# Kernel tuning notes

Hardware: AMD Instinct MI355X
Metric: run time of the kernel (lower is better)

The kernel has to match this reference:

```python
import jax, jax.numpy as jnp
import numpy as np

HEADS, DHEAD = 8, 32
INNER = HEADS * DHEAD  # 256


def _conv3x3(x, w, b):
    y = jax.lax.conv_general_dilated(x, w, (1, 1), ((1, 1), (1, 1)),
                                     dimension_numbers=('NCHW', 'OIHW', 'NCHW'))
    return y + b[None, :, None, None]


def _conv1x1(x, w, b):
    return jnp.einsum('oc,bchw->bohw', w, x) + b[None, :, None, None]


def setup_inputs() -> dict:
    key = jax.random.key(0)
    ks = jax.random.split(key, 16)
    s = 0.02
    return {
        'x': jax.random.normal(ks[0], (2, 256, 48, 48), jnp.float32),
        'luma': jax.random.uniform(ks[1], (2, 1, 48, 48), jnp.float32),
        'w_qkv': jax.random.normal(ks[2], (768, 256), jnp.float32) * s,
        'b_qkv': jax.random.normal(ks[3], (768,), jnp.float32) * s,
        'w_proj': jax.random.normal(ks[4], (256, 256), jnp.float32) * s,
        'b_proj': jax.random.normal(ks[5], (256,), jnp.float32) * s,
        'w_c1': jax.random.normal(ks[6], (128, 1, 3, 3), jnp.float32) * s,
        'b_c1': jax.random.normal(ks[7], (128,), jnp.float32) * s,
        'w_c2': jax.random.normal(ks[8], (128, 128, 3, 3), jnp.float32) * s,
        'b_c2': jax.random.normal(ks[9], (128,), jnp.float32) * s,
        'w_g': jax.random.normal(ks[10], (256, 128), jnp.float32) * s,
        'b_g': jax.random.normal(ks[11], (256,), jnp.float32) * s,
        'w_bt': jax.random.normal(ks[12], (256, 128), jnp.float32) * s,
        'b_bt': jax.random.normal(ks[13], (256,), jnp.float32) * s,
        'alpha': jax.random.normal(ks[14], (), jnp.float32) * 0.1,
    }


def reference(x, luma, w_qkv, b_qkv, w_proj, b_proj, w_c1, b_c1, w_c2, b_c2,
              w_g, b_g, w_bt, b_bt, alpha):
    B, C, H, W = x.shape
    N = H * W
    scale = DHEAD ** -0.5

    def to_heads(t):  # [B, h*d, H, W] -> [B, h, N, d]
        return t.reshape(B, HEADS, DHEAD, N).transpose(0, 1, 3, 2)

    qkv = _conv1x1(x, w_qkv, b_qkv)
    q = to_heads(qkv[:, 0 * INNER:1 * INNER])
    k = to_heads(qkv[:, 1 * INNER:2 * INNER])
    v = to_heads(qkv[:, 2 * INNER:3 * INNER])

    # luma conditioning net
    h = jax.nn.relu(_conv3x3(luma, w_c1, b_c1))
    h = jax.nn.relu(_conv3x3(h, w_c2, b_c2))
    gamma = to_heads(_conv1x1(h, w_g, b_g))
    beta = to_heads(_conv1x1(h, w_bt, b_bt))
    q = gamma * q + beta
    k = gamma * k + beta
    v = gamma * v + beta

    # luminance bias: avg_pool2d(3, stride=1, pad=1, count_include_pad=True)
    invL = 1.0 - luma
    invL = jax.lax.reduce_window(invL, 0.0, jax.lax.add, (1, 1, 3, 3), (1, 1, 1, 1),
                                 ((0, 0), (0, 0), (1, 1), (1, 1))) / 9.0
    invL = invL.reshape(B, N)
    invL = invL - invL.mean(axis=-1, keepdims=True)
    q = q + alpha * invL[:, None, :, None]

    attn = jax.nn.softmax(jnp.einsum('bhid,bhjd->bhij', q, k) * scale, axis=-1)
    out = jnp.einsum('bhij,bhjd->bhid', attn, v)
    out = out.transpose(0, 1, 3, 2).reshape(B, INNER, H, W)
    return _conv1x1(out, w_proj, b_proj)
```

## Files before the change

kernel.cpp:

```cpp
#include <hip/hip_runtime.h>
#include <hip/hip_bf16.h>
#include <math.h>
#include <string.h>

#define NB 2
#define NN 2304
#define NHEADS 8
#define DH 32
#define KPW 576

typedef __attribute__((ext_vector_type(8))) short v8s;
typedef __attribute__((ext_vector_type(4))) float v4f;

__device__ inline unsigned short f2b(float f) {
    unsigned u = __builtin_bit_cast(unsigned, f);
    unsigned r = u + 0x7FFFu + ((u >> 16) & 1u);
    return (unsigned short)(r >> 16);
}
__device__ inline float b2f(short s) {
    unsigned u = ((unsigned)(unsigned short)s) << 16;
    return __builtin_bit_cast(float, u);
}
__device__ inline unsigned pk2(float a, float b) {
    __hip_bfloat162 h = __float22bfloat162_rn(make_float2(a, b));
    unsigned r;
    memcpy(&r, &h, sizeof(r));
    return r;
}
__device__ inline float blo(unsigned u) { return __builtin_bit_cast(float, u << 16); }
__device__ inline float bhi(unsigned u) { return __builtin_bit_cast(float, u & 0xffff0000u); }

__global__ void k_prep(const float* __restrict__ wc1, const float* __restrict__ wc2,
                       const float* __restrict__ wqkv, const float* __restrict__ wg,
                       const float* __restrict__ wbt, const float* __restrict__ wproj,
                       float* __restrict__ twc1, short* __restrict__ tc2b,
                       short* __restrict__ wqkvb, short* __restrict__ wgb,
                       short* __restrict__ wbtb, short* __restrict__ wprojb,
                       float* __restrict__ vsum) {
    int i = blockIdx.x * 256 + threadIdx.x;
    if (i < 16 * DH) vsum[i] = 0.f;
    if (i < 9 * 128) {
        int k = i / 128, c = i % 128;
        twc1[i] = wc1[c * 9 + k];
    }
    if (i < 9 * 128 * 128) {
        int s = i / (128 * 128);
        int rem = i % (128 * 128);
        int o = rem / 128, ic = rem % 128;
        tc2b[i] = (short)f2b(wc2[(o * 128 + ic) * 9 + s]);
    }
    if (i < 768 * 256) wqkvb[i] = (short)f2b(wqkv[i]);
    if (i < 256 * 128) { wgb[i] = (short)f2b(wg[i]); wbtb[i] = (short)f2b(wbt[i]); }
    if (i < 256 * 256) wprojb[i] = (short)f2b(wproj[i]);
}

__global__ void k_conv1(const float* __restrict__ luma, const float* __restrict__ twc1,
                        const float* __restrict__ bc1, short* __restrict__ h1p) {
    int c = threadIdx.x & 127;
    int p = (blockIdx.x % 1250) * 2 + (threadIdx.x >> 7);
    int b = blockIdx.x / 1250;
    int py = p / 50, px = p % 50;
    float val = 0.f;
    if (py >= 1 && py <= 48 && px >= 1 && px <= 48) {
        int y = py - 1, x = px - 1;
        const float* lb = luma + b * NN;
        float acc = bc1[c];
#pragma unroll
        for (int ky = 0; ky < 3; ++ky) {
            int yy = y + ky - 1;
            if (yy < 0 || yy >= 48) continue;
#pragma unroll
            for (int kx = 0; kx < 3; ++kx) {
                int xx = x + kx - 1;
                if (xx < 0 || xx >= 48) continue;
                acc += twc1[(ky * 3 + kx) * 128 + c] * lb[yy * 48 + xx];
            }
        }
        val = fmaxf(acc, 0.f);
    }
    h1p[((size_t)b * 2500 + p) * 128 + c] = (short)f2b(val);
}

__global__ void k_xt(const float* __restrict__ x, short* __restrict__ xt,
                     const float* __restrict__ luma, float* __restrict__ invl) {
    __shared__ unsigned short lds[64 * 66];
    __shared__ float red[256];
    int blk = blockIdx.x;
    if (blk >= NB * 144) {
        int b = blk - NB * 144;
        const float* lb = luma + b * NN;
        float pooled[9];
        float local = 0.f;
#pragma unroll
        for (int it = 0; it < 9; ++it) {
            int n = it * 256 + threadIdx.x;
            int y = n / 48, xx0 = n % 48;
            float s = 0.f;
            for (int ky = 0; ky < 3; ++ky) {
                int yy = y + ky - 1;
                if (yy < 0 || yy >= 48) continue;
                for (int kx = 0; kx < 3; ++kx) {
                    int xx = xx0 + kx - 1;
                    if (xx < 0 || xx >= 48) continue;
                    s += 1.f - lb[yy * 48 + xx];
                }
            }
            s *= (1.f / 9.f);
            pooled[it] = s;
            local += s;
        }
        red[threadIdx.x] = local;
        __syncthreads();
        for (int off = 128; off > 0; off >>= 1) {
            if (threadIdx.x < off) red[threadIdx.x] += red[threadIdx.x + off];
            __syncthreads();
        }
        float mean = red[0] * (1.f / NN);
#pragma unroll
        for (int it = 0; it < 9; ++it) {
            int n = it * 256 + threadIdx.x;
            invl[b * NN + n] = pooled[it] - mean;
        }
        return;
    }
    int nt = blk % 36, ct = (blk / 36) % 4, b = blk / 144;
    int n0 = nt * 64, c0 = ct * 64;
    int nc = threadIdx.x & 63, cr = threadIdx.x >> 6;
#pragma unroll
    for (int i = 0; i < 16; ++i) {
        int cs = i * 4 + cr;
        float v = x[((size_t)b * 256 + c0 + cs) * NN + n0 + nc];
        lds[nc * 66 + cs] = f2b(v);
    }
    __syncthreads();
    int cc = threadIdx.x & 31, nr = threadIdx.x >> 5;
    unsigned* xt2 = (unsigned*)xt;
#pragma unroll
    for (int j = 0; j < 8; ++j) {
        int ns = j * 8 + nr;
        unsigned w = *(unsigned*)&lds[ns * 66 + 2 * cc];
        xt2[(((size_t)b * NN + n0 + ns) * 256 + c0) / 2 + cc] = w;
    }
}

__global__ __launch_bounds__(64) void k_conv2m(const short* __restrict__ h1p,
                                               const short* __restrict__ tc2b,
                                               const float* __restrict__ bc2,
                                               short* __restrict__ h2t) {
    int lane = threadIdx.x, l15 = lane & 15, g = lane >> 4;
    int blk = blockIdx.x;
    int ntg = blk % 72, ot = (blk / 72) % 8, b = blk / (72 * 8);
    int nta = ntg * 2, ntb = ntg * 2 + 1;
    int ya = nta / 3, xa = (nta % 3) * 16;
    int yb = ntb / 3, xb = (ntb % 3) * 16;
    int p0a = (ya + 1) * 50 + xa + 1;
    int p0b = (yb + 1) * 50 + xb + 1;
    const short* hb = h1p + (size_t)b * 2500 * 128;

    v4f acca = {0.f,0.f,0.f,0.f}, accb = acca;
#pragma unroll
    for (int s = 0; s < 9; ++s) {
        int dp = (s / 3 - 1) * 50 + (s % 3 - 1);
#pragma unroll
        for (int kk = 0; kk < 4; ++kk) {
            v8s A = *(const v8s*)(tc2b + ((size_t)(s * 128 + ot * 16 + l15)) * 128 + kk * 32 + 8 * g);
            v8s Ba = *(const v8s*)(hb + (size_t)(p0a + dp + l15) * 128 + kk * 32 + 8 * g);
            v8s Bb = *(const v8s*)(hb + (size_t)(p0b + dp + l15) * 128 + kk * 32 + 8 * g);
            acca = __builtin_amdgcn_mfma_f32_16x16x32_bf16(A, Ba, acca, 0, 0, 0);
            accb = __builtin_amdgcn_mfma_f32_16x16x32_bf16(A, Bb, accb, 0, 0, 0);
        }
    }
    v4f bias = *(const v4f*)&bc2[ot * 16 + 4 * g];
    int na = ya * 48 + xa + l15, nb = yb * 48 + xb + l15;
    uint2 wa, wb;
    wa.x = pk2(fmaxf(acca[0] + bias[0], 0.f), fmaxf(acca[1] + bias[1], 0.f));
    wa.y = pk2(fmaxf(acca[2] + bias[2], 0.f), fmaxf(acca[3] + bias[3], 0.f));
    wb.x = pk2(fmaxf(accb[0] + bias[0], 0.f), fmaxf(accb[1] + bias[1], 0.f));
    wb.y = pk2(fmaxf(accb[2] + bias[2], 0.f), fmaxf(accb[3] + bias[3], 0.f));
    *(uint2*)&h2t[((size_t)b * NN + na) * 128 + ot * 16 + 4 * g] = wa;
    *(uint2*)&h2t[((size_t)b * NN + nb) * 128 + ot * 16 + 4 * g] = wb;
}

__global__ __launch_bounds__(64) void k_gbm(const short* __restrict__ h2t,
                                            const short* __restrict__ wgb,
                                            const short* __restrict__ wbtb,
                                            const float* __restrict__ bg,
                                            const float* __restrict__ bbt,
                                            short* __restrict__ gtb, short* __restrict__ bttb) {
    int lane = threadIdx.x, l15 = lane & 15, g = lane >> 4;
    int blk = blockIdx.x;
    int ntg = blk % 72, ot = (blk / 72) % 16, b = blk / (72 * 16);
    int na0 = ntg * 32, nb0 = ntg * 32 + 16;
    const short* hb = h2t + (size_t)b * NN * 128;

    v4f ga = {0.f,0.f,0.f,0.f}, gb = ga, ta = ga, tb = ga;
#pragma unroll
    for (int kk = 0; kk < 4; ++kk) {
        v8s Ag = *(const v8s*)(wgb + (size_t)(ot * 16 + l15) * 128 + kk * 32 + 8 * g);
        v8s At = *(const v8s*)(wbtb + (size_t)(ot * 16 + l15) * 128 + kk * 32 + 8 * g);
        v8s Ba = *(const v8s*)(hb + (size_t)(na0 + l15) * 128 + kk * 32 + 8 * g);
        v8s Bb = *(const v8s*)(hb + (size_t)(nb0 + l15) * 128 + kk * 32 + 8 * g);
        ga = __builtin_amdgcn_mfma_f32_16x16x32_bf16(Ag, Ba, ga, 0, 0, 0);
        gb = __builtin_amdgcn_mfma_f32_16x16x32_bf16(Ag, Bb, gb, 0, 0, 0);
        ta = __builtin_amdgcn_mfma_f32_16x16x32_bf16(At, Ba, ta, 0, 0, 0);
        tb = __builtin_amdgcn_mfma_f32_16x16x32_bf16(At, Bb, tb, 0, 0, 0);
    }
    v4f bgv = *(const v4f*)&bg[ot * 16 + 4 * g];
    v4f bbv = *(const v4f*)&bbt[ot * 16 + 4 * g];
    size_t oa = ((size_t)b * NN + na0 + l15) * 256 + ot * 16 + 4 * g;
    size_t ob = ((size_t)b * NN + nb0 + l15) * 256 + ot * 16 + 4 * g;
    uint2 w;
    w.x = pk2(ga[0] + bgv[0], ga[1] + bgv[1]); w.y = pk2(ga[2] + bgv[2], ga[3] + bgv[3]);
    *(uint2*)&gtb[oa] = w;
    w.x = pk2(gb[0] + bgv[0], gb[1] + bgv[1]); w.y = pk2(gb[2] + bgv[2], gb[3] + bgv[3]);
    *(uint2*)&gtb[ob] = w;
    w.x = pk2(ta[0] + bbv[0], ta[1] + bbv[1]); w.y = pk2(ta[2] + bbv[2], ta[3] + bbv[3]);
    *(uint2*)&bttb[oa] = w;
    w.x = pk2(tb[0] + bbv[0], tb[1] + bbv[1]); w.y = pk2(tb[2] + bbv[2], tb[3] + bbv[3]);
    *(uint2*)&bttb[ob] = w;
}

__global__ __launch_bounds__(64) void k_qkvm(const short* __restrict__ xt,
                                             const short* __restrict__ wqkvb,
                                             const float* __restrict__ bqkv,
                                             const short* __restrict__ gtb,
                                             const short* __restrict__ bttb,
                                             const float* __restrict__ invl,
                                             const float* __restrict__ alpha_p,
                                             short* __restrict__ qb, short* __restrict__ kb,
                                             short* __restrict__ vraw) {
    int lane = threadIdx.x, l15 = lane & 15, g = lane >> 4;
    int blk = blockIdx.x;
    int ntg = blk % 72, ot = (blk / 72) % 48, b = blk / (72 * 48);
    int na0 = ntg * 32, nb0 = ntg * 32 + 16;
    const short* xb = xt + (size_t)b * NN * 256;

    v4f acca = {0.f,0.f,0.f,0.f}, accb = acca;
#pragma unroll
    for (int kk = 0; kk < 8; ++kk) {
        v8s A = *(const v8s*)(wqkvb + (size_t)(ot * 16 + l15) * 256 + kk * 32 + 8 * g);
        v8s Ba = *(const v8s*)(xb + (size_t)(na0 + l15) * 256 + kk * 32 + 8 * g);
        v8s Bb = *(const v8s*)(xb + (size_t)(nb0 + l15) * 256 + kk * 32 + 8 * g);
        acca = __builtin_amdgcn_mfma_f32_16x16x32_bf16(A, Ba, acca, 0, 0, 0);
        accb = __builtin_amdgcn_mfma_f32_16x16x32_bf16(A, Bb, accb, 0, 0, 0);
    }
    int which = ot >> 4;
    int cbase = (ot & 15) * 16 + 4 * g;
    int h = cbase >> 5, dbase = cbase & 31;
    v4f bias = *(const v4f*)&bqkv[which * 256 + cbase];
    const float scale = 0.25503486f;
    float alpha = *alpha_p;
    short* dst = (which == 0) ? qb : (which == 1) ? kb : vraw;
#pragma unroll
    for (int t = 0; t < 2; ++t) {
        int n = (t == 0 ? na0 : nb0) + l15;
        v4f acc = (t == 0) ? acca : accb;
        uint2 gg = *(const uint2*)&gtb[((size_t)b * NN + n) * 256 + cbase];
        uint2 tt = *(const uint2*)&bttb[((size_t)b * NN + n) * 256 + cbase];
        float iv = (which == 0) ? alpha * invl[b * NN + n] : 0.f;
        float v0 = blo(gg.x) * (acc[0] + bias[0]) + blo(tt.x);
        float v1 = bhi(gg.x) * (acc[1] + bias[1]) + bhi(tt.x);
        float v2 = blo(gg.y) * (acc[2] + bias[2]) + blo(tt.y);
        float v3 = bhi(gg.y) * (acc[3] + bias[3]) + bhi(tt.y);
        if (which == 0) {
            v0 = (v0 + iv) * scale; v1 = (v1 + iv) * scale;
            v2 = (v2 + iv) * scale; v3 = (v3 + iv) * scale;
        }
        uint2 w;
        w.x = pk2(v0, v1);
        w.y = pk2(v2, v3);
        *(uint2*)&dst[(((size_t)b * NHEADS + h) * NN + n) * DH + dbase] = w;
    }
}

__global__ void k_vt(const short* __restrict__ vraw, short* __restrict__ vtb,
                     float* __restrict__ vsum) {
    __shared__ unsigned short lds[64 * 34];
    int bh = blockIdx.x / 36, nc = blockIdx.x % 36;
    int n0 = nc * 64;
    int dpair = threadIdx.x & 15, nsub = (threadIdx.x >> 4) & 15;
    const unsigned* vr2 = (const unsigned*)vraw;
#pragma unroll
    for (int i = 0; i < 4; ++i) {
        int ns = i * 16 + nsub;
        unsigned v = vr2[((size_t)bh * NN + n0 + ns) * 16 + dpair];
        *(unsigned*)&lds[ns * 34 + 2 * dpair] = v;
    }
    __syncthreads();
    int pn = threadIdx.x & 31, drow = threadIdx.x >> 5;
    int kb0 = n0 >> 5;
    unsigned* vtb2 = (unsigned*)vtb;
#pragma unroll
    for (int j = 0; j < 4; ++j) {
        int d = j * 8 + drow;
        unsigned lo = lds[(2 * pn) * 34 + d];
        unsigned hi = lds[(2 * pn + 1) * 34 + d];
        vtb2[(((size_t)bh * 72 + kb0 + (pn >> 4)) * 32 + d) * 16 + (pn & 15)] = lo | (hi << 16);
    }
    if (threadIdx.x < 32) {
        int d = threadIdx.x;
        float s = 0.f;
        for (int ns = 0; ns < 64; ++ns) s += b2f((short)lds[ns * 34 + d]);
        atomicAdd(&vsum[bh * DH + d], s);
    }
}

__global__ __launch_bounds__(256) void k_attn2(const short* __restrict__ qb,
                                               const short* __restrict__ kbuf,
                                               const short* __restrict__ vtb,
                                               const float* __restrict__ vsum,
                                               short* __restrict__ aotb) {
    __shared__ short plds[4][32 * 40];
    __shared__ float acc_lds[4][32][36];
    __shared__ float ps_lds[4][32];
    int tid = threadIdx.x;
    int w = tid >> 6, lane = tid & 63;
    int l15 = lane & 15, g = lane >> 4;
    int blk = blockIdx.x;
    int logical = (blk & 7) * 144 + (blk >> 3);
    int qt = logical % 72, bh = logical / 72;
    int qbase = qt * 32;

    const short* qp = qb + ((size_t)bh * NN + qbase) * DH;
    const short* kp = kbuf + ((size_t)bh * NN + w * KPW) * DH;
    const short* vp = vtb + ((size_t)bh * 72 + w * (KPW / 32)) * 1024;

    v8s q0 = *(const v8s*)(qp + l15 * DH + 8 * g);
    v8s q1 = *(const v8s*)(qp + (16 + l15) * DH + 8 * g);

    const short one_b = (short)0x3F80;
    const v8s ones = {one_b, one_b, one_b, one_b, one_b, one_b, one_b, one_b};

    v4f acc00 = {0.f,0.f,0.f,0.f}, acc01 = acc00, acc10 = acc00, acc11 = acc00;
    v4f acc_ps0 = {0.f,0.f,0.f,0.f}, acc_ps1 = acc_ps0;
    short* pw = plds[w];

    for (int it = 0; it < KPW / 32; ++it) {
        const short* kpi = kp + it * 32 * DH;
        v8s ka0 = *(const v8s*)(kpi + l15 * DH + 8 * g);
        v8s ka1 = *(const v8s*)(kpi + (16 + l15) * DH + 8 * g);
        v4f s00 = __builtin_amdgcn_mfma_f32_16x16x32_bf16(ka0, q0, (v4f){0.f,0.f,0.f,0.f}, 0, 0, 0);
        v4f s01 = __builtin_amdgcn_mfma_f32_16x16x32_bf16(ka0, q1, (v4f){0.f,0.f,0.f,0.f}, 0, 0, 0);
        v4f s10 = __builtin_amdgcn_mfma_f32_16x16x32_bf16(ka1, q0, (v4f){0.f,0.f,0.f,0.f}, 0, 0, 0);
        v4f s11 = __builtin_amdgcn_mfma_f32_16x16x32_bf16(ka1, q1, (v4f){0.f,0.f,0.f,0.f}, 0, 0, 0);

#define DOFRAG(S, QTL, KT)                                                       \
        {                                                                        \
            float p0 = __builtin_amdgcn_exp2f((S)[0]) - 1.f;                     \
            float p1 = __builtin_amdgcn_exp2f((S)[1]) - 1.f;                     \
            float p2 = __builtin_amdgcn_exp2f((S)[2]) - 1.f;                     \
            float p3 = __builtin_amdgcn_exp2f((S)[3]) - 1.f;                     \
            uint2 wv;                                                            \
            wv.x = pk2(p0, p1);                                                  \
            wv.y = pk2(p2, p3);                                                  \
            *(uint2*)((char*)pw + ((QTL) * 16 + l15) * 80 + ((KT) * 16 + 4 * g) * 2) = wv; \
        }
        DOFRAG(s00, 0, 0)
        DOFRAG(s01, 1, 0)
        DOFRAG(s10, 0, 1)
        DOFRAG(s11, 1, 1)
#undef DOFRAG
        v8s pa0 = *(v8s*)((char*)pw + l15 * 80 + 16 * g);
        v8s pa1 = *(v8s*)((char*)pw + (16 + l15) * 80 + 16 * g);
        const short* vpi = vp + it * 1024;
        v8s vb0 = *(const v8s*)(vpi + l15 * 32 + 8 * g);
        v8s vb1 = *(const v8s*)(vpi + (16 + l15) * 32 + 8 * g);
        acc00 = __builtin_amdgcn_mfma_f32_16x16x32_bf16(pa0, vb0, acc00, 0, 0, 0);
        acc01 = __builtin_amdgcn_mfma_f32_16x16x32_bf16(pa0, vb1, acc01, 0, 0, 0);
        acc10 = __builtin_amdgcn_mfma_f32_16x16x32_bf16(pa1, vb0, acc10, 0, 0, 0);
        acc11 = __builtin_amdgcn_mfma_f32_16x16x32_bf16(pa1, vb1, acc11, 0, 0, 0);
        acc_ps0 = __builtin_amdgcn_mfma_f32_16x16x32_bf16(pa0, ones, acc_ps0, 0, 0, 0);
        acc_ps1 = __builtin_amdgcn_mfma_f32_16x16x32_bf16(pa1, ones, acc_ps1, 0, 0, 0);
    }

    if (l15 == 0) {
#pragma unroll
        for (int r = 0; r < 4; ++r) {
            ps_lds[w][4 * g + r] = acc_ps0[r];
            ps_lds[w][16 + 4 * g + r] = acc_ps1[r];
        }
    }

#define DUMP(ACC, QTL, DT)                                                         \
    {                                                                              \
        _Pragma("unroll")                                                          \
        for (int r = 0; r < 4; ++r)                                                \
            acc_lds[w][(QTL) * 16 + 4 * g + r][(DT) * 16 + l15] = (ACC)[r];        \
    }
    DUMP(acc00, 0, 0)
    DUMP(acc01, 1, 0)
    DUMP(acc10, 0, 1)
    DUMP(acc11, 1, 1)
#undef DUMP
    __syncthreads();

    int q = tid >> 3, d0 = (tid & 7) * 4;
    float L = (float)NN;
    v4f a = {0.f, 0.f, 0.f, 0.f};
#pragma unroll
    for (int wv = 0; wv < 4; ++wv) {
        L += ps_lds[wv][q];
        v4f t4 = *(v4f*)&acc_lds[wv][q][d0];
        a[0] += t4[0]; a[1] += t4[1]; a[2] += t4[2]; a[3] += t4[3];
    }
    const float* vs = vsum + bh * DH + d0;
    float rl = 1.f / L;
    uint2 o;
    o.x = pk2((a[0] + vs[0]) * rl, (a[1] + vs[1]) * rl);
    o.y = pk2((a[2] + vs[2]) * rl, (a[3] + vs[3]) * rl);
    int b = bh >> 3, h = bh & 7;
    *(uint2*)&aotb[((size_t)b * NN + qbase + q) * 256 + h * DH + d0] = o;
}

__global__ __launch_bounds__(64) void k_projm(const short* __restrict__ aotb,
                                              const short* __restrict__ wprojb,
                                              const float* __restrict__ bproj,
                                              float* __restrict__ out) {
    int lane = threadIdx.x, l15 = lane & 15, g = lane >> 4;
    int blk = blockIdx.x;
    int ntg = blk % 72, ot = (blk / 72) % 16, b = blk / (72 * 16);
    int na0 = ntg * 32, nb0 = ntg * 32 + 16;
    const short* ab = aotb + (size_t)b * NN * 256;

    v4f acca = {0.f,0.f,0.f,0.f}, accb = acca;
#pragma unroll
    for (int kk = 0; kk < 8; ++kk) {
        v8s A = *(const v8s*)(wprojb + (size_t)(ot * 16 + l15) * 256 + kk * 32 + 8 * g);
        v8s Ba = *(const v8s*)(ab + (size_t)(na0 + l15) * 256 + kk * 32 + 8 * g);
        v8s Bb = *(const v8s*)(ab + (size_t)(nb0 + l15) * 256 + kk * 32 + 8 * g);
        acca = __builtin_amdgcn_mfma_f32_16x16x32_bf16(A, Ba, acca, 0, 0, 0);
        accb = __builtin_amdgcn_mfma_f32_16x16x32_bf16(A, Bb, accb, 0, 0, 0);
    }
    v4f bias = *(const v4f*)&bproj[ot * 16 + 4 * g];
#pragma unroll
    for (int r = 0; r < 4; ++r) {
        int o = ot * 16 + 4 * g + r;
        out[((size_t)b * 256 + o) * NN + na0 + l15] = acca[r] + bias[r];
        out[((size_t)b * 256 + o) * NN + nb0 + l15] = accb[r] + bias[r];
    }
}

extern "C" void kernel_launch(void* const* d_in, const int* in_sizes, int n_in,
                              void* d_out, int out_size, void* d_ws, size_t ws_size,
                              hipStream_t stream) {
    const float* x     = (const float*)d_in[0];
    const float* luma  = (const float*)d_in[1];
    const float* wqkv  = (const float*)d_in[2];
    const float* bqkv  = (const float*)d_in[3];
    const float* wproj = (const float*)d_in[4];
    const float* bproj = (const float*)d_in[5];
    const float* wc1   = (const float*)d_in[6];
    const float* bc1   = (const float*)d_in[7];
    const float* wc2   = (const float*)d_in[8];
    const float* bc2   = (const float*)d_in[9];
    const float* wg    = (const float*)d_in[10];
    const float* bg    = (const float*)d_in[11];
    const float* wbt   = (const float*)d_in[12];
    const float* bbt   = (const float*)d_in[13];
    const float* alpha = (const float*)d_in[14];
    float* out = (float*)d_out;

    float* ws = (float*)d_ws;
    size_t off = 0;
    float* twc1 = ws + off;            off += 9 * 128;
    short* tc2b = (short*)(ws + off);  off += 9 * 128 * 128 / 2;
    short* wqkvb = (short*)(ws + off); off += 768 * 256 / 2;
    short* wgb = (short*)(ws + off);   off += 256 * 128 / 2;
    short* wbtb = (short*)(ws + off);  off += 256 * 128 / 2;
    short* wprojb = (short*)(ws + off); off += 256 * 256 / 2;
    short* h1p = (short*)(ws + off);   off += NB * 2500 * 128 / 2;
    short* xt = (short*)(ws + off);    off += NB * NN * 256 / 2;
    short* h2t = (short*)(ws + off);   off += NB * NN * 128 / 2;
    short* gtb = (short*)(ws + off);   off += NB * NN * 256 / 2;
    short* bttb = (short*)(ws + off);  off += NB * NN * 256 / 2;
    float* invl = ws + off;            off += NB * NN;
    short* qbb = (short*)(ws + off);   off += 16 * NN * DH / 2;
    short* kbb = (short*)(ws + off);   off += 16 * NN * DH / 2;
    short* vraw = (short*)(ws + off);  off += 16 * NN * DH / 2;
    short* vtb = (short*)(ws + off);   off += 16 * NN * DH / 2;
    float* vsum = ws + off;            off += 16 * DH;
    short* aotb = (short*)(ws + off);  off += NB * NN * 256 / 2;
    (void)ws_size; (void)in_sizes; (void)n_in; (void)out_size;

    k_prep<<<768, 256, 0, stream>>>(wc1, wc2, wqkv, wg, wbt, wproj,
                                    twc1, tc2b, wqkvb, wgb, wbtb, wprojb, vsum);
    k_conv1<<<NB * 1250, 256, 0, stream>>>(luma, twc1, bc1, h1p);
    k_xt<<<NB * 144 + NB, 256, 0, stream>>>(x, xt, luma, invl);
    k_conv2m<<<NB * 8 * 72, 64, 0, stream>>>(h1p, tc2b, bc2, h2t);
    k_gbm<<<NB * 16 * 72, 64, 0, stream>>>(h2t, wgb, wbtb, bg, bbt, gtb, bttb);
    k_qkvm<<<NB * 48 * 72, 64, 0, stream>>>(xt, wqkvb, bqkv, gtb, bttb, invl, alpha,
                                            qbb, kbb, vraw);
    k_vt<<<16 * 36, 256, 0, stream>>>(vraw, vtb, vsum);
    k_attn2<<<16 * 72, 256, 0, stream>>>(qbb, kbb, vtb, vsum, aotb);
    k_projm<<<NB * 16 * 72, 64, 0, stream>>>(aotb, wprojb, bproj, out);
}
```

Baseline: 113.6 us.

## Fuse conv1 into front kernel and enlarge MFMA tiles across GEMMs and attention

Merges the conv1 and x-transpose/pool kernels into a single launch. Each wave in conv2, gamma/beta, qkv and proj now computes four 16-column tiles, and qkv/proj also cover two output tiles, so every A/B fragment load feeds more MFMAs. Attention processes 64 queries per block instead of 32, reusing each K/V fragment across four query fragments, and raises wave priority around the PV MFMAs. In exchange there are fewer blocks (lower occupancy and parallelism), more registers per wave, and more LDS in attention.

```diff
diff --git a/kernel.cpp b/kernel.cpp
--- a/kernel.cpp
+++ b/kernel.cpp
@@ -54,38 +54,40 @@
     if (i < 256 * 256) wprojb[i] = (short)f2b(wproj[i]);
 }
 
-__global__ void k_conv1(const float* __restrict__ luma, const float* __restrict__ twc1,
-                        const float* __restrict__ bc1, short* __restrict__ h1p) {
-    int c = threadIdx.x & 127;
-    int p = (blockIdx.x % 1250) * 2 + (threadIdx.x >> 7);
-    int b = blockIdx.x / 1250;
-    int py = p / 50, px = p % 50;
-    float val = 0.f;
-    if (py >= 1 && py <= 48 && px >= 1 && px <= 48) {
-        int y = py - 1, x = px - 1;
-        const float* lb = luma + b * NN;
-        float acc = bc1[c];
-#pragma unroll
-        for (int ky = 0; ky < 3; ++ky) {
-            int yy = y + ky - 1;
-            if (yy < 0 || yy >= 48) continue;
-#pragma unroll
-            for (int kx = 0; kx < 3; ++kx) {
-                int xx = x + kx - 1;
-                if (xx < 0 || xx >= 48) continue;
-                acc += twc1[(ky * 3 + kx) * 128 + c] * lb[yy * 48 + xx];
-            }
-        }
-        val = fmaxf(acc, 0.f);
-    }
-    h1p[((size_t)b * 2500 + p) * 128 + c] = (short)f2b(val);
-}
-
-__global__ void k_xt(const float* __restrict__ x, short* __restrict__ xt,
-                     const float* __restrict__ luma, float* __restrict__ invl) {
+__global__ void k_front(const float* __restrict__ x, short* __restrict__ xt,
+                        const float* __restrict__ luma, float* __restrict__ invl,
+                        const float* __restrict__ twc1, const float* __restrict__ bc1,
+                        short* __restrict__ h1p) {
     __shared__ unsigned short lds[64 * 66];
     __shared__ float red[256];
     int blk = blockIdx.x;
+    if (blk >= NB * 144 + NB) {
+        int cb = blk - (NB * 144 + NB);
+        int c = threadIdx.x & 127;
+        int p = (cb % 1250) * 2 + (threadIdx.x >> 7);
+        int b = cb / 1250;
+        int py = p / 50, px = p % 50;
+        float val = 0.f;
+        if (py >= 1 && py <= 48 && px >= 1 && px <= 48) {
+            int y = py - 1, xx0 = px - 1;
+            const float* lb = luma + b * NN;
+            float acc = bc1[c];
+#pragma unroll
+            for (int ky = 0; ky < 3; ++ky) {
+                int yy = y + ky - 1;
+                if (yy < 0 || yy >= 48) continue;
+#pragma unroll
+                for (int kx = 0; kx < 3; ++kx) {
+                    int xx = xx0 + kx - 1;
+                    if (xx < 0 || xx >= 48) continue;
+                    acc += twc1[(ky * 3 + kx) * 128 + c] * lb[yy * 48 + xx];
+                }
+            }
+            val = fmaxf(acc, 0.f);
+        }
+        h1p[((size_t)b * 2500 + p) * 128 + c] = (short)f2b(val);
+        return;
+    }
     if (blk >= NB * 144) {
         int b = blk - NB * 144;
         const float* lb = luma + b * NN;
@@ -149,36 +151,39 @@
                                                short* __restrict__ h2t) {
     int lane = threadIdx.x, l15 = lane & 15, g = lane >> 4;
     int blk = blockIdx.x;
-    int ntg = blk % 72, ot = (blk / 72) % 8, b = blk / (72 * 8);
-    int nta = ntg * 2, ntb = ntg * 2 + 1;
-    int ya = nta / 3, xa = (nta % 3) * 16;
-    int yb = ntb / 3, xb = (ntb % 3) * 16;
-    int p0a = (ya + 1) * 50 + xa + 1;
-    int p0b = (yb + 1) * 50 + xb + 1;
+    int ntg = blk % 36, ot = (blk / 36) % 8, b = blk / (36 * 8);
+    int p0[4], na[4];
+#pragma unroll
+    for (int j = 0; j < 4; ++j) {
+        int nt = ntg * 4 + j;
+        int y = nt / 3, xx = (nt % 3) * 16;
+        p0[j] = (y + 1) * 50 + xx + 1;
+        na[j] = y * 48 + xx + l15;
+    }
     const short* hb = h1p + (size_t)b * 2500 * 128;
 
-    v4f acca = {0.f,0.f,0.f,0.f}, accb = acca;
+    v4f acc[4] = {{0.f,0.f,0.f,0.f},{0.f,0.f,0.f,0.f},{0.f,0.f,0.f,0.f},{0.f,0.f,0.f,0.f}};
 #pragma unroll
     for (int s = 0; s < 9; ++s) {
         int dp = (s / 3 - 1) * 50 + (s % 3 - 1);
 #pragma unroll
         for (int kk = 0; kk < 4; ++kk) {
             v8s A = *(const v8s*)(tc2b + ((size_t)(s * 128 + ot * 16 + l15)) * 128 + kk * 32 + 8 * g);
-            v8s Ba = *(const v8s*)(hb + (size_t)(p0a + dp + l15) * 128 + kk * 32 + 8 * g);
-            v8s Bb = *(const v8s*)(hb + (size_t)(p0b + dp + l15) * 128 + kk * 32 + 8 * g);
-            acca = __builtin_amdgcn_mfma_f32_16x16x32_bf16(A, Ba, acca, 0, 0, 0);
-            accb = __builtin_amdgcn_mfma_f32_16x16x32_bf16(A, Bb, accb, 0, 0, 0);
+#pragma unroll
+            for (int j = 0; j < 4; ++j) {
+                v8s B = *(const v8s*)(hb + (size_t)(p0[j] + dp + l15) * 128 + kk * 32 + 8 * g);
+                acc[j] = __builtin_amdgcn_mfma_f32_16x16x32_bf16(A, B, acc[j], 0, 0, 0);
+            }
         }
     }
     v4f bias = *(const v4f*)&bc2[ot * 16 + 4 * g];
-    int na = ya * 48 + xa + l15, nb = yb * 48 + xb + l15;
-    uint2 wa, wb;
-    wa.x = pk2(fmaxf(acca[0] + bias[0], 0.f), fmaxf(acca[1] + bias[1], 0.f));
-    wa.y = pk2(fmaxf(acca[2] + bias[2], 0.f), fmaxf(acca[3] + bias[3], 0.f));
-    wb.x = pk2(fmaxf(accb[0] + bias[0], 0.f), fmaxf(accb[1] + bias[1], 0.f));
-    wb.y = pk2(fmaxf(accb[2] + bias[2], 0.f), fmaxf(accb[3] + bias[3], 0.f));
-    *(uint2*)&h2t[((size_t)b * NN + na) * 128 + ot * 16 + 4 * g] = wa;
-    *(uint2*)&h2t[((size_t)b * NN + nb) * 128 + ot * 16 + 4 * g] = wb;
+#pragma unroll
+    for (int j = 0; j < 4; ++j) {
+        uint2 w;
+        w.x = pk2(fmaxf(acc[j][0] + bias[0], 0.f), fmaxf(acc[j][1] + bias[1], 0.f));
+        w.y = pk2(fmaxf(acc[j][2] + bias[2], 0.f), fmaxf(acc[j][3] + bias[3], 0.f));
+        *(uint2*)&h2t[((size_t)b * NN + na[j]) * 128 + ot * 16 + 4 * g] = w;
+    }
 }
 
 __global__ __launch_bounds__(64) void k_gbm(const short* __restrict__ h2t,
@@ -189,35 +194,36 @@
                                             short* __restrict__ gtb, short* __restrict__ bttb) {
     int lane = threadIdx.x, l15 = lane & 15, g = lane >> 4;
     int blk = blockIdx.x;
-    int ntg = blk % 72, ot = (blk / 72) % 16, b = blk / (72 * 16);
-    int na0 = ntg * 32, nb0 = ntg * 32 + 16;
+    int ntg = blk % 36, ot = (blk / 36) % 16, b = blk / (36 * 16);
+    int n0 = ntg * 64;
     const short* hb = h2t + (size_t)b * NN * 128;
 
-    v4f ga = {0.f,0.f,0.f,0.f}, gb = ga, ta = ga, tb = ga;
+    v4f ga[4] = {{0.f,0.f,0.f,0.f},{0.f,0.f,0.f,0.f},{0.f,0.f,0.f,0.f},{0.f,0.f,0.f,0.f}};
+    v4f ta[4] = {{0.f,0.f,0.f,0.f},{0.f,0.f,0.f,0.f},{0.f,0.f,0.f,0.f},{0.f,0.f,0.f,0.f}};
 #pragma unroll
     for (int kk = 0; kk < 4; ++kk) {
         v8s Ag = *(const v8s*)(wgb + (size_t)(ot * 16 + l15) * 128 + kk * 32 + 8 * g);
         v8s At = *(const v8s*)(wbtb + (size_t)(ot * 16 + l15) * 128 + kk * 32 + 8 * g);
-        v8s Ba = *(const v8s*)(hb + (size_t)(na0 + l15) * 128 + kk * 32 + 8 * g);
-        v8s Bb = *(const v8s*)(hb + (size_t)(nb0 + l15) * 128 + kk * 32 + 8 * g);
-        ga = __builtin_amdgcn_mfma_f32_16x16x32_bf16(Ag, Ba, ga, 0, 0, 0);
-        gb = __builtin_amdgcn_mfma_f32_16x16x32_bf16(Ag, Bb, gb, 0, 0, 0);
-        ta = __builtin_amdgcn_mfma_f32_16x16x32_bf16(At, Ba, ta, 0, 0, 0);
-        tb = __builtin_amdgcn_mfma_f32_16x16x32_bf16(At, Bb, tb, 0, 0, 0);
+#pragma unroll
+        for (int j = 0; j < 4; ++j) {
+            v8s B = *(const v8s*)(hb + (size_t)(n0 + j * 16 + l15) * 128 + kk * 32 + 8 * g);
+            ga[j] = __builtin_amdgcn_mfma_f32_16x16x32_bf16(Ag, B, ga[j], 0, 0, 0);
+            ta[j] = __builtin_amdgcn_mfma_f32_16x16x32_bf16(At, B, ta[j], 0, 0, 0);
+        }
     }
     v4f bgv = *(const v4f*)&bg[ot * 16 + 4 * g];
     v4f bbv = *(const v4f*)&bbt[ot * 16 + 4 * g];
-    size_t oa = ((size_t)b * NN + na0 + l15) * 256 + ot * 16 + 4 * g;
-    size_t ob = ((size_t)b * NN + nb0 + l15) * 256 + ot * 16 + 4 * g;
-    uint2 w;
-    w.x = pk2(ga[0] + bgv[0], ga[1] + bgv[1]); w.y = pk2(ga[2] + bgv[2], ga[3] + bgv[3]);
-    *(uint2*)&gtb[oa] = w;
-    w.x = pk2(gb[0] + bgv[0], gb[1] + bgv[1]); w.y = pk2(gb[2] + bgv[2], gb[3] + bgv[3]);
-    *(uint2*)&gtb[ob] = w;
-    w.x = pk2(ta[0] + bbv[0], ta[1] + bbv[1]); w.y = pk2(ta[2] + bbv[2], ta[3] + bbv[3]);
-    *(uint2*)&bttb[oa] = w;
-    w.x = pk2(tb[0] + bbv[0], tb[1] + bbv[1]); w.y = pk2(tb[2] + bbv[2], tb[3] + bbv[3]);
-    *(uint2*)&bttb[ob] = w;
+#pragma unroll
+    for (int j = 0; j < 4; ++j) {
+        size_t o = ((size_t)b * NN + n0 + j * 16 + l15) * 256 + ot * 16 + 4 * g;
+        uint2 w;
+        w.x = pk2(ga[j][0] + bgv[0], ga[j][1] + bgv[1]);
+        w.y = pk2(ga[j][2] + bgv[2], ga[j][3] + bgv[3]);
+        *(uint2*)&gtb[o] = w;
+        w.x = pk2(ta[j][0] + bbv[0], ta[j][1] + bbv[1]);
+        w.y = pk2(ta[j][2] + bbv[2], ta[j][3] + bbv[3]);
+        *(uint2*)&bttb[o] = w;
+    }
 }
 
 __global__ __launch_bounds__(64) void k_qkvm(const short* __restrict__ xt,
@@ -231,45 +237,56 @@
                                              short* __restrict__ vraw) {
     int lane = threadIdx.x, l15 = lane & 15, g = lane >> 4;
     int blk = blockIdx.x;
-    int ntg = blk % 72, ot = (blk / 72) % 48, b = blk / (72 * 48);
-    int na0 = ntg * 32, nb0 = ntg * 32 + 16;
+    int ntg = blk % 36, otg = (blk / 36) % 24, b = blk / (36 * 24);
+    int n0 = ntg * 64;
     const short* xb = xt + (size_t)b * NN * 256;
 
-    v4f acca = {0.f,0.f,0.f,0.f}, accb = acca;
+    v4f acc[2][4];
+#pragma unroll
+    for (int oa = 0; oa < 2; ++oa)
+#pragma unroll
+        for (int j = 0; j < 4; ++j) acc[oa][j] = (v4f){0.f, 0.f, 0.f, 0.f};
 #pragma unroll
     for (int kk = 0; kk < 8; ++kk) {
-        v8s A = *(const v8s*)(wqkvb + (size_t)(ot * 16 + l15) * 256 + kk * 32 + 8 * g);
-        v8s Ba = *(const v8s*)(xb + (size_t)(na0 + l15) * 256 + kk * 32 + 8 * g);
-        v8s Bb = *(const v8s*)(xb + (size_t)(nb0 + l15) * 256 + kk * 32 + 8 * g);
-        acca = __builtin_amdgcn_mfma_f32_16x16x32_bf16(A, Ba, acca, 0, 0, 0);
-        accb = __builtin_amdgcn_mfma_f32_16x16x32_bf16(A, Bb, accb, 0, 0, 0);
-    }
-    int which = ot >> 4;
-    int cbase = (ot & 15) * 16 + 4 * g;
-    int h = cbase >> 5, dbase = cbase & 31;
-    v4f bias = *(const v4f*)&bqkv[which * 256 + cbase];
+        v8s A0 = *(const v8s*)(wqkvb + (size_t)(otg * 32 + l15) * 256 + kk * 32 + 8 * g);
+        v8s A1 = *(const v8s*)(wqkvb + (size_t)(otg * 32 + 16 + l15) * 256 + kk * 32 + 8 * g);
+#pragma unroll
+        for (int j = 0; j < 4; ++j) {
+            v8s B = *(const v8s*)(xb + (size_t)(n0 + j * 16 + l15) * 256 + kk * 32 + 8 * g);
+            acc[0][j] = __builtin_amdgcn_mfma_f32_16x16x32_bf16(A0, B, acc[0][j], 0, 0, 0);
+            acc[1][j] = __builtin_amdgcn_mfma_f32_16x16x32_bf16(A1, B, acc[1][j], 0, 0, 0);
+        }
+    }
     const float scale = 0.25503486f;
     float alpha = *alpha_p;
-    short* dst = (which == 0) ? qb : (which == 1) ? kb : vraw;
-#pragma unroll
-    for (int t = 0; t < 2; ++t) {
-        int n = (t == 0 ? na0 : nb0) + l15;
-        v4f acc = (t == 0) ? acca : accb;
-        uint2 gg = *(const uint2*)&gtb[((size_t)b * NN + n) * 256 + cbase];
-        uint2 tt = *(const uint2*)&bttb[((size_t)b * NN + n) * 256 + cbase];
-        float iv = (which == 0) ? alpha * invl[b * NN + n] : 0.f;
-        float v0 = blo(gg.x) * (acc[0] + bias[0]) + blo(tt.x);
-        float v1 = bhi(gg.x) * (acc[1] + bias[1]) + bhi(tt.x);
-        float v2 = blo(gg.y) * (acc[2] + bias[2]) + blo(tt.y);
-        float v3 = bhi(gg.y) * (acc[3] + bias[3]) + bhi(tt.y);
-        if (which == 0) {
-            v0 = (v0 + iv) * scale; v1 = (v1 + iv) * scale;
-            v2 = (v2 + iv) * scale; v3 = (v3 + iv) * scale;
-        }
-        uint2 w;
-        w.x = pk2(v0, v1);
-        w.y = pk2(v2, v3);
-        *(uint2*)&dst[(((size_t)b * NHEADS + h) * NN + n) * DH + dbase] = w;
+#pragma unroll
+    for (int oa = 0; oa < 2; ++oa) {
+        int ocb = otg * 32 + oa * 16;
+        int which = ocb >> 8;
+        int cbase = (ocb & 255) + 4 * g;
+        int h = cbase >> 5, dbase = cbase & 31;
+        v4f bias = *(const v4f*)&bqkv[ocb + 4 * g];
+        short* dst = (which == 0) ? qb : (which == 1) ? kb : vraw;
+#pragma unroll
+        for (int j = 0; j < 4; ++j) {
+            int n = n0 + j * 16 + l15;
+            v4f a = acc[oa][j];
+            uint2 gg = *(const uint2*)&gtb[((size_t)b * NN + n) * 256 + cbase];
+            uint2 tt = *(const uint2*)&bttb[((size_t)b * NN + n) * 256 + cbase];
+            float iv = (which == 0) ? alpha * invl[b * NN + n] : 0.f;
+            float v0 = blo(gg.x) * (a[0] + bias[0]) + blo(tt.x);
+            float v1 = bhi(gg.x) * (a[1] + bias[1]) + bhi(tt.x);
+            float v2 = blo(gg.y) * (a[2] + bias[2]) + blo(tt.y);
+            float v3 = bhi(gg.y) * (a[3] + bias[3]) + bhi(tt.y);
+            if (which == 0) {
+                v0 = (v0 + iv) * scale; v1 = (v1 + iv) * scale;
+                v2 = (v2 + iv) * scale; v3 = (v3 + iv) * scale;
+            }
+            uint2 w;
+            w.x = pk2(v0, v1);
+            w.y = pk2(v2, v3);
+            *(uint2*)&dst[(((size_t)b * NHEADS + h) * NN + n) * DH + dbase] = w;
+        }
     }
 }
 
@@ -310,16 +327,16 @@
                                                const short* __restrict__ vtb,
                                                const float* __restrict__ vsum,
                                                short* __restrict__ aotb) {
-    __shared__ short plds[4][32 * 40];
-    __shared__ float acc_lds[4][32][36];
-    __shared__ float ps_lds[4][32];
+    __shared__ short plds[4][64 * 40];
+    __shared__ float acc_lds[4][64][35];
+    __shared__ float ps_lds[4][64];
     int tid = threadIdx.x;
     int w = tid >> 6, lane = tid & 63;
     int l15 = lane & 15, g = lane >> 4;
     int blk = blockIdx.x;
-    int logical = (blk & 7) * 144 + (blk >> 3);
-    int qt = logical % 72, bh = logical / 72;
-    int qbase = qt * 32;
+    int logical = (blk & 7) * 72 + (blk >> 3);
+    int qt = logical % 36, bh = logical / 36;
+    int qbase = qt * 64;
 
     const short* qp = qb + ((size_t)bh * NN + qbase) * DH;
     const short* kp = kbuf + ((size_t)bh * NN + w * KPW) * DH;
@@ -327,12 +344,18 @@
 
     v8s q0 = *(const v8s*)(qp + l15 * DH + 8 * g);
     v8s q1 = *(const v8s*)(qp + (16 + l15) * DH + 8 * g);
+    v8s q2 = *(const v8s*)(qp + (32 + l15) * DH + 8 * g);
+    v8s q3 = *(const v8s*)(qp + (48 + l15) * DH + 8 * g);
 
     const short one_b = (short)0x3F80;
     const v8s ones = {one_b, one_b, one_b, one_b, one_b, one_b, one_b, one_b};
 
-    v4f acc00 = {0.f,0.f,0.f,0.f}, acc01 = acc00, acc10 = acc00, acc11 = acc00;
-    v4f acc_ps0 = {0.f,0.f,0.f,0.f}, acc_ps1 = acc_ps0;
+    v4f acc[2][4];
+#pragma unroll
+    for (int dt = 0; dt < 2; ++dt)
+#pragma unroll
+        for (int qf = 0; qf < 4; ++qf) acc[dt][qf] = (v4f){0.f, 0.f, 0.f, 0.f};
+    v4f ps[4] = {{0.f,0.f,0.f,0.f},{0.f,0.f,0.f,0.f},{0.f,0.f,0.f,0.f},{0.f,0.f,0.f,0.f}};
     short* pw = plds[w];
 
     for (int it = 0; it < KPW / 32; ++it) {
@@ -341,10 +364,14 @@
         v8s ka1 = *(const v8s*)(kpi + (16 + l15) * DH + 8 * g);
         v4f s00 = __builtin_amdgcn_mfma_f32_16x16x32_bf16(ka0, q0, (v4f){0.f,0.f,0.f,0.f}, 0, 0, 0);
         v4f s01 = __builtin_amdgcn_mfma_f32_16x16x32_bf16(ka0, q1, (v4f){0.f,0.f,0.f,0.f}, 0, 0, 0);
+        v4f s02 = __builtin_amdgcn_mfma_f32_16x16x32_bf16(ka0, q2, (v4f){0.f,0.f,0.f,0.f}, 0, 0, 0);
+        v4f s03 = __builtin_amdgcn_mfma_f32_16x16x32_bf16(ka0, q3, (v4f){0.f,0.f,0.f,0.f}, 0, 0, 0);
         v4f s10 = __builtin_amdgcn_mfma_f32_16x16x32_bf16(ka1, q0, (v4f){0.f,0.f,0.f,0.f}, 0, 0, 0);
         v4f s11 = __builtin_amdgcn_mfma_f32_16x16x32_bf16(ka1, q1, (v4f){0.f,0.f,0.f,0.f}, 0, 0, 0);
-
-#define DOFRAG(S, QTL, KT)                                                       \
+        v4f s12 = __builtin_amdgcn_mfma_f32_16x16x32_bf16(ka1, q2, (v4f){0.f,0.f,0.f,0.f}, 0, 0, 0);
+        v4f s13 = __builtin_amdgcn_mfma_f32_16x16x32_bf16(ka1, q3, (v4f){0.f,0.f,0.f,0.f}, 0, 0, 0);
+
+#define DOFRAG(S, QF, KT)                                                        \
         {                                                                        \
             float p0 = __builtin_amdgcn_exp2f((S)[0]) - 1.f;                     \
             float p1 = __builtin_amdgcn_exp2f((S)[1]) - 1.f;                     \
@@ -353,63 +380,75 @@
             uint2 wv;                                                            \
             wv.x = pk2(p0, p1);                                                  \
             wv.y = pk2(p2, p3);                                                  \
-            *(uint2*)((char*)pw + ((QTL) * 16 + l15) * 80 + ((KT) * 16 + 4 * g) * 2) = wv; \
+            *(uint2*)((char*)pw + ((QF) * 16 + l15) * 80 + ((KT) * 16 + 4 * g) * 2) = wv; \
         }
         DOFRAG(s00, 0, 0)
         DOFRAG(s01, 1, 0)
+        DOFRAG(s02, 2, 0)
+        DOFRAG(s03, 3, 0)
         DOFRAG(s10, 0, 1)
         DOFRAG(s11, 1, 1)
+        DOFRAG(s12, 2, 1)
+        DOFRAG(s13, 3, 1)
 #undef DOFRAG
         v8s pa0 = *(v8s*)((char*)pw + l15 * 80 + 16 * g);
         v8s pa1 = *(v8s*)((char*)pw + (16 + l15) * 80 + 16 * g);
+        v8s pa2 = *(v8s*)((char*)pw + (32 + l15) * 80 + 16 * g);
+        v8s pa3 = *(v8s*)((char*)pw + (48 + l15) * 80 + 16 * g);
         const short* vpi = vp + it * 1024;
         v8s vb0 = *(const v8s*)(vpi + l15 * 32 + 8 * g);
         v8s vb1 = *(const v8s*)(vpi + (16 + l15) * 32 + 8 * g);
-        acc00 = __builtin_amdgcn_mfma_f32_16x16x32_bf16(pa0, vb0, acc00, 0, 0, 0);
-        acc01 = __builtin_amdgcn_mfma_f32_16x16x32_bf16(pa0, vb1, acc01, 0, 0, 0);
-        acc10 = __builtin_amdgcn_mfma_f32_16x16x32_bf16(pa1, vb0, acc10, 0, 0, 0);
-        acc11 = __builtin_amdgcn_mfma_f32_16x16x32_bf16(pa1, vb1, acc11, 0, 0, 0);
-        acc_ps0 = __builtin_amdgcn_mfma_f32_16x16x32_bf16(pa0, ones, acc_ps0, 0, 0, 0);
-        acc_ps1 = __builtin_amdgcn_mfma_f32_16x16x32_bf16(pa1, ones, acc_ps1, 0, 0, 0);
+        __builtin_amdgcn_s_setprio(1);
+        acc[0][0] = __builtin_amdgcn_mfma_f32_16x16x32_bf16(pa0, vb0, acc[0][0], 0, 0, 0);
+        acc[1][0] = __builtin_amdgcn_mfma_f32_16x16x32_bf16(pa0, vb1, acc[1][0], 0, 0, 0);
+        acc[0][1] = __builtin_amdgcn_mfma_f32_16x16x32_bf16(pa1, vb0, acc[0][1], 0, 0, 0);
+        acc[1][1] = __builtin_amdgcn_mfma_f32_16x16x32_bf16(pa1, vb1, acc[1][1], 0, 0, 0);
+        acc[0][2] = __builtin_amdgcn_mfma_f32_16x16x32_bf16(pa2, vb0, acc[0][2], 0, 0, 0);
+        acc[1][2] = __builtin_amdgcn_mfma_f32_16x16x32_bf16(pa2, vb1, acc[1][2], 0, 0, 0);
+        acc[0][3] = __builtin_amdgcn_mfma_f32_16x16x32_bf16(pa3, vb0, acc[0][3], 0, 0, 0);
+        acc[1][3] = __builtin_amdgcn_mfma_f32_16x16x32_bf16(pa3, vb1, acc[1][3], 0, 0, 0);
+        ps[0] = __builtin_amdgcn_mfma_f32_16x16x32_bf16(pa0, ones, ps[0], 0, 0, 0);
+        ps[1] = __builtin_amdgcn_mfma_f32_16x16x32_bf16(pa1, ones, ps[1], 0, 0, 0);
+        ps[2] = __builtin_amdgcn_mfma_f32_16x16x32_bf16(pa2, ones, ps[2], 0, 0, 0);
+        ps[3] = __builtin_amdgcn_mfma_f32_16x16x32_bf16(pa3, ones, ps[3], 0, 0, 0);
+        __builtin_amdgcn_s_setprio(0);
     }
 
     if (l15 == 0) {
 #pragma unroll
-        for (int r = 0; r < 4; ++r) {
-            ps_lds[w][4 * g + r] = acc_ps0[r];
-            ps_lds[w][16 + 4 * g + r] = acc_ps1[r];
-        }
-    }
-
-#define DUMP(ACC, QTL, DT)                                                         \
-    {                                                                              \
-        _Pragma("unroll")                                                          \
-        for (int r = 0; r < 4; ++r)                                                \
-            acc_lds[w][(QTL) * 16 + 4 * g + r][(DT) * 16 + l15] = (ACC)[r];        \
-    }
-    DUMP(acc00, 0, 0)
-    DUMP(acc01, 1, 0)
-    DUMP(acc10, 0, 1)
-    DUMP(acc11, 1, 1)
-#undef DUMP
+        for (int qf = 0; qf < 4; ++qf)
+#pragma unroll
+            for (int r = 0; r < 4; ++r)
+                ps_lds[w][qf * 16 + 4 * g + r] = ps[qf][r];
+    }
+#pragma unroll
+    for (int qf = 0; qf < 4; ++qf)
+#pragma unroll
+        for (int dt = 0; dt < 2; ++dt)
+#pragma unroll
+            for (int r = 0; r < 4; ++r)
+                acc_lds[w][qf * 16 + 4 * g + r][dt * 16 + l15] = acc[dt][qf][r];
     __syncthreads();
 
-    int q = tid >> 3, d0 = (tid & 7) * 4;
+    int q = tid >> 2, d0 = (tid & 3) * 8;
     float L = (float)NN;
-    v4f a = {0.f, 0.f, 0.f, 0.f};
+    float a[8] = {0.f, 0.f, 0.f, 0.f, 0.f, 0.f, 0.f, 0.f};
 #pragma unroll
     for (int wv = 0; wv < 4; ++wv) {
         L += ps_lds[wv][q];
-        v4f t4 = *(v4f*)&acc_lds[wv][q][d0];
-        a[0] += t4[0]; a[1] += t4[1]; a[2] += t4[2]; a[3] += t4[3];
+        const float* row = &acc_lds[wv][q][d0];
+#pragma unroll
+        for (int j = 0; j < 8; ++j) a[j] += row[j];
     }
     const float* vs = vsum + bh * DH + d0;
     float rl = 1.f / L;
-    uint2 o;
+    uint4 o;
     o.x = pk2((a[0] + vs[0]) * rl, (a[1] + vs[1]) * rl);
     o.y = pk2((a[2] + vs[2]) * rl, (a[3] + vs[3]) * rl);
+    o.z = pk2((a[4] + vs[4]) * rl, (a[5] + vs[5]) * rl);
+    o.w = pk2((a[6] + vs[6]) * rl, (a[7] + vs[7]) * rl);
     int b = bh >> 3, h = bh & 7;
-    *(uint2*)&aotb[((size_t)b * NN + qbase + q) * 256 + h * DH + d0] = o;
+    *(uint4*)&aotb[((size_t)b * NN + qbase + q) * 256 + h * DH + d0] = o;
 }
 
 __global__ __launch_bounds__(64) void k_projm(const short* __restrict__ aotb,
@@ -418,25 +457,37 @@
                                               float* __restrict__ out) {
     int lane = threadIdx.x, l15 = lane & 15, g = lane >> 4;
     int blk = blockIdx.x;
-    int ntg = blk % 72, ot = (blk / 72) % 16, b = blk / (72 * 16);
-    int na0 = ntg * 32, nb0 = ntg * 32 + 16;
+    int ntg = blk % 36, otg = (blk / 36) % 8, b = blk / (36 * 8);
+    int n0 = ntg * 64;
     const short* ab = aotb + (size_t)b * NN * 256;
 
-    v4f acca = {0.f,0.f,0.f,0.f}, accb = acca;
+    v4f acc[2][4];
+#pragma unroll
+    for (int oa = 0; oa < 2; ++oa)
+#pragma unroll
+        for (int j = 0; j < 4; ++j) acc[oa][j] = (v4f){0.f, 0.f, 0.f, 0.f};
 #pragma unroll
     for (int kk = 0; kk < 8; ++kk) {
-        v8s A = *(const v8s*)(wprojb + (size_t)(ot * 16 + l15) * 256 + kk * 32 + 8 * g);
-        v8s Ba = *(const v8s*)(ab + (size_t)(na0 + l15) * 256 + kk * 32 + 8 * g);
-        v8s Bb = *(const v8s*)(ab + (size_t)(nb0 + l15) * 256 + kk * 32 + 8 * g);
-        acca = __builtin_amdgcn_mfma_f32_16x16x32_bf16(A, Ba, acca, 0, 0, 0);
-        accb = __builtin_amdgcn_mfma_f32_16x16x32_bf16(A, Bb, accb, 0, 0, 0);
-    }
-    v4f bias = *(const v4f*)&bproj[ot * 16 + 4 * g];
-#pragma unroll
-    for (int r = 0; r < 4; ++r) {
-        int o = ot * 16 + 4 * g + r;
-        out[((size_t)b * 256 + o) * NN + na0 + l15] = acca[r] + bias[r];
-        out[((size_t)b * 256 + o) * NN + nb0 + l15] = accb[r] + bias[r];
+        v8s A0 = *(const v8s*)(wprojb + (size_t)(otg * 32 + l15) * 256 + kk * 32 + 8 * g);
+        v8s A1 = *(const v8s*)(wprojb + (size_t)(otg * 32 + 16 + l15) * 256 + kk * 32 + 8 * g);
+#pragma unroll
+        for (int j = 0; j < 4; ++j) {
+            v8s B = *(const v8s*)(ab + (size_t)(n0 + j * 16 + l15) * 256 + kk * 32 + 8 * g);
+            acc[0][j] = __builtin_amdgcn_mfma_f32_16x16x32_bf16(A0, B, acc[0][j], 0, 0, 0);
+            acc[1][j] = __builtin_amdgcn_mfma_f32_16x16x32_bf16(A1, B, acc[1][j], 0, 0, 0);
+        }
+    }
+#pragma unroll
+    for (int oa = 0; oa < 2; ++oa) {
+        v4f bias = *(const v4f*)&bproj[otg * 32 + oa * 16 + 4 * g];
+#pragma unroll
+        for (int j = 0; j < 4; ++j) {
+#pragma unroll
+            for (int r = 0; r < 4; ++r) {
+                int o = otg * 32 + oa * 16 + 4 * g + r;
+                out[((size_t)b * 256 + o) * NN + n0 + j * 16 + l15] = acc[oa][j][r] + bias[r];
+            }
+        }
     }
 }
 
@@ -484,13 +535,12 @@
 
     k_prep<<<768, 256, 0, stream>>>(wc1, wc2, wqkv, wg, wbt, wproj,
                                     twc1, tc2b, wqkvb, wgb, wbtb, wprojb, vsum);
-    k_conv1<<<NB * 1250, 256, 0, stream>>>(luma, twc1, bc1, h1p);
-    k_xt<<<NB * 144 + NB, 256, 0, stream>>>(x, xt, luma, invl);
-    k_conv2m<<<NB * 8 * 72, 64, 0, stream>>>(h1p, tc2b, bc2, h2t);
-    k_gbm<<<NB * 16 * 72, 64, 0, stream>>>(h2t, wgb, wbtb, bg, bbt, gtb, bttb);
-    k_qkvm<<<NB * 48 * 72, 64, 0, stream>>>(xt, wqkvb, bqkv, gtb, bttb, invl, alpha,
+    k_front<<<NB * 144 + NB + NB * 1250, 256, 0, stream>>>(x, xt, luma, invl, twc1, bc1, h1p);
+    k_conv2m<<<NB * 8 * 36, 64, 0, stream>>>(h1p, tc2b, bc2, h2t);
+    k_gbm<<<NB * 16 * 36, 64, 0, stream>>>(h2t, wgb, wbtb, bg, bbt, gtb, bttb);
+    k_qkvm<<<NB * 24 * 36, 64, 0, stream>>>(xt, wqkvb, bqkv, gtb, bttb, invl, alpha,
                                             qbb, kbb, vraw);
     k_vt<<<16 * 36, 256, 0, stream>>>(vraw, vtb, vsum);
-    k_attn2<<<16 * 72, 256, 0, stream>>>(qbb, kbb, vtb, vsum, aotb);
-    k_projm<<<NB * 16 * 72, 64, 0, stream>>>(aotb, wprojb, bproj, out);
-}
+    k_attn2<<<576, 256, 0, stream>>>(qbb, kbb, vtb, vsum, aotb);
+    k_projm<<<NB * 8 * 36, 64, 0, stream>>>(aotb, wprojb, bproj, out);
+}
```

Result: faster. 111.0 us (-2.3%).
